# Kernel tuning notes

Measured on AMD Instinct MI355X. Metric: run time of the kernel, lower is better.

Reference implementation:

```python
import jax, jax.numpy as jnp
import numpy as np

K = 3
K2 = K * K


def conv2d(x, w, b, stride=1, pad=0):
    y = jax.lax.conv_general_dilated(
        x, w, (stride, stride), [(pad, pad), (pad, pad)],
        dimension_numbers=('NCHW', 'OIHW', 'NCHW'))
    return y + b[None, :, None, None]


def bilinear_gather(x, ys, xs):
    # x: [B,C,H,W]; ys,xs: [B,K2,H,W] float coords; zero outside bounds (torchvision deform_conv2d semantics)
    B, C, H, W = x.shape
    y0 = jnp.floor(ys)
    x0 = jnp.floor(xs)
    fy = (ys - y0)[:, None]  # [B,1,K2,H,W]
    fx = (xs - x0)[:, None]
    xf = x.reshape(B, C, H * W)

    def gather(yc, xc):
        valid = (yc >= 0) & (yc <= H - 1) & (xc >= 0) & (xc <= W - 1)
        yi = jnp.clip(yc, 0, H - 1).astype(jnp.int32)
        xi = jnp.clip(xc, 0, W - 1).astype(jnp.int32)
        idx = (yi * W + xi).reshape(B, 1, -1)
        g = jnp.take_along_axis(xf, idx, axis=2).reshape(B, C, K2, H, W)
        return g * valid[:, None].astype(x.dtype)

    g00 = gather(y0, x0)
    g01 = gather(y0, x0 + 1)
    g10 = gather(y0 + 1, x0)
    g11 = gather(y0 + 1, x0 + 1)
    return (g00 * (1 - fy) * (1 - fx) + g01 * (1 - fy) * fx
            + g10 * fy * (1 - fx) + g11 * fy * fx)


def deform_conv(x, w_off, b_off, w, b):
    # DCNv1: offsets predicted by a regular 3x3 conv, then 3x3 conv over bilinearly sampled taps
    B, C, H, W = x.shape
    pad = 1
    off = conv2d(x, w_off, b_off, pad=pad).reshape(B, K2, 2, H, W)  # (dy,dx) per tap
    ky, kx = jnp.meshgrid(jnp.arange(K), jnp.arange(K), indexing='ij')
    base_y = jnp.arange(H)[None, None, :, None] + (ky.reshape(K2) - pad)[None, :, None, None]
    base_x = jnp.arange(W)[None, None, None, :] + (kx.reshape(K2) - pad)[None, :, None, None]
    ys = base_y + off[:, :, 0]
    xs = base_x + off[:, :, 1]
    samples = bilinear_gather(x, ys, xs)  # [B,C,K2,H,W]
    out = jnp.einsum('bckhw,ock->bohw', samples, w.reshape(w.shape[0], C, K2))
    return out + b[None, :, None, None]


def band_high_mask(h, w):
    y, x = jnp.meshgrid(jnp.arange(h), jnp.arange(w), indexing='ij')
    d = jnp.sqrt(((y - h // 2) ** 2 + (x - w // 2) ** 2).astype(jnp.float32))
    return (d > h // 16).astype(jnp.float32)


def reference(x, w1, b1, ws, bs, wb, bb, woff, boff, wreg, breg, w2, b2):
    B, Cin, Hx, Wx = x.shape
    c0 = conv2d(x, w1, b1)                                  # 1x1 reduce
    c1 = conv2d(c0, ws, bs, stride=2, pad=0)                # 3x3 s2 p0 -> 111x111
    c1 = jax.lax.reduce_window(c1, -jnp.inf, jax.lax.max,
                               (1, 1, 7, 7), (1, 1, 3, 3), 'VALID')  # -> 35x35
    f = jnp.fft.fftshift(jnp.fft.fft2(c1, axes=(-2, -1)), axes=(-2, -1))
    mag = jnp.abs(f)
    phase = jnp.angle(f)
    h, w = mag.shape[-2], mag.shape[-1]
    hb = mag * band_high_mask(h, w)
    for l in range(3):  # fixed structural loop over the 3 DCN+ReLU blocks
        hb = jax.nn.relu(deform_conv(hb, woff[l], boff[l], wreg[l], breg[l]))
    rec = jax.lax.complex(hb * jnp.cos(phase), hb * jnp.sin(phase))
    rec = jnp.real(jnp.fft.ifft2(jnp.fft.ifftshift(rec, axes=(-2, -1)), axes=(-2, -1)))
    up = jax.image.resize(rec, (B, rec.shape[1], Hx, Wx), method='bilinear')  # align_corners=False
    c2 = jax.nn.sigmoid(conv2d(conv2d(c0, wb, bb) + up, w2, b2))
    return x * c2


def setup_inputs():
    key = jax.random.key(0)
    ks = jax.random.split(key, 8)
    B, Cin, H, W = 4, 256, 224, 224
    Cr = Cin // 8
    f32 = jnp.float32
    x = jax.random.normal(ks[0], (B, Cin, H, W), f32)
    w1 = jax.random.normal(ks[1], (Cr, Cin, 1, 1), f32) * 0.05
    b1 = jnp.zeros((Cr,), f32)
    ws = jax.random.normal(ks[2], (Cr, Cr, 3, 3), f32) * 0.05
    bs = jnp.zeros((Cr,), f32)
    wb = jax.random.normal(ks[3], (Cr, Cr, 1, 1), f32) * 0.05
    bb = jnp.zeros((Cr,), f32)
    woff = jax.random.normal(ks[4], (3, 2 * K2, Cr, 3, 3), f32) * 0.002  # small -> moderate offsets
    boff = jnp.zeros((3, 2 * K2), f32)
    wreg = jax.random.normal(ks[5], (3, Cr, Cr, 3, 3), f32) * 0.05
    breg = jnp.zeros((3, Cr), f32)
    w2 = jax.random.normal(ks[6], (Cin, Cr, 1, 1), f32) * 0.05
    b2 = jnp.zeros((Cin,), f32)
    return dict(x=x, w1=w1, b1=b1, ws=ws, bs=bs, wb=wb, bb=bb,
                woff=woff, boff=boff, wreg=wreg, breg=breg, w2=w2, b2=b2)
```

## Files before the change

### kernel.cpp

```cpp
#include <hip/hip_runtime.h>
#include <math.h>

#define PI_F 3.14159265358979323846f

#define BATCH 4
#define CIN 256
#define CR 32
#define H0 224
#define HW0 (224*224)
#define H1 111
#define HW1 (111*111)
#define HS 35
#define HWS (35*35)

typedef short bf16x8 __attribute__((ext_vector_type(8)));
typedef float f32x4 __attribute__((ext_vector_type(4)));
typedef unsigned int u32x4 __attribute__((ext_vector_type(4)));

__device__ inline unsigned pack2(float a, float b) {
  unsigned ua = __builtin_bit_cast(unsigned, a);
  unsigned ub = __builtin_bit_cast(unsigned, b);
  return ((ua + 0x8000u) >> 16) | (((ub + 0x8000u) >> 16) << 16);
}

__device__ inline bf16x8 pack8(const float f[8]) {
  u32x4 u;
  u[0] = pack2(f[0], f[1]);
  u[1] = pack2(f[2], f[3]);
  u[2] = pack2(f[4], f[5]);
  u[3] = pack2(f[6], f[7]);
  return __builtin_bit_cast(bf16x8, u);
}

__global__ __launch_bounds__(256) void k_prep(
    const float* __restrict__ w1, const float* __restrict__ b1,
    const float* __restrict__ wb, const float* __restrict__ bb,
    float* __restrict__ Wcat, float* __restrict__ bias_v) {
  __shared__ float wbl[32 * 32];
  int t = threadIdx.x;
  for (int i = t; i < 1024; i += 256) wbl[i] = wb[i];
  __syncthreads();
  float col[32];
#pragma unroll
  for (int m = 0; m < 32; ++m) col[m] = w1[m * CIN + t];
#pragma unroll
  for (int o = 0; o < 32; ++o) {
    float s = 0.f;
#pragma unroll
    for (int m = 0; m < 32; ++m) s = fmaf(wbl[o * 32 + m], col[m], s);
    Wcat[o * CIN + t] = s;
  }
  if (t < 32) {
    float s = bb[t];
#pragma unroll
    for (int m = 0; m < 32; ++m) s = fmaf(wbl[t * 32 + m], b1[m], s);
    bias_v[t] = s;
  }
}

__global__ __launch_bounds__(256) void k_conv1x1(
    const float* __restrict__ x, const float* __restrict__ w1,
    const float* __restrict__ b1, const float* __restrict__ Wcat,
    const float* __restrict__ bias_v,
    float* __restrict__ c0, float* __restrict__ v0) {
  int tid = threadIdx.x, lane = tid & 63, wid = tid >> 6;
  int l15 = lane & 15, lg = lane >> 4;
  int pxg = blockIdx.x * 256 + wid * 64;
  int b = pxg / HW0, p0 = pxg % HW0;
  f32x4 acc[4][4];
#pragma unroll
  for (int ct = 0; ct < 4; ++ct)
#pragma unroll
    for (int pt = 0; pt < 4; ++pt)
#pragma unroll
      for (int r = 0; r < 4; ++r) acc[ct][pt][r] = 0.f;
  const float* xb = x + (size_t)b * CIN * HW0 + p0 + l15;
  for (int ks = 0; ks < 8; ++ks) {
    bf16x8 Bf[4];
#pragma unroll
    for (int pt = 0; pt < 4; ++pt) {
      const float* xp = xb + (size_t)(ks * 32 + lg * 8) * HW0 + pt * 16;
      float f[8];
#pragma unroll
      for (int j = 0; j < 8; ++j) f[j] = xp[(size_t)j * HW0];
      Bf[pt] = pack8(f);
    }
    bf16x8 A[4];
#pragma unroll
    for (int ct = 0; ct < 4; ++ct) {
      const float* base = (ct < 2)
          ? w1 + (ct * 16 + l15) * CIN
          : Wcat + ((ct - 2) * 16 + l15) * CIN;
      const float* wr = base + ks * 32 + lg * 8;
      float f[8];
      float4 a0 = *reinterpret_cast<const float4*>(wr);
      float4 a1 = *reinterpret_cast<const float4*>(wr + 4);
      f[0]=a0.x; f[1]=a0.y; f[2]=a0.z; f[3]=a0.w;
      f[4]=a1.x; f[5]=a1.y; f[6]=a1.z; f[7]=a1.w;
      A[ct] = pack8(f);
    }
#pragma unroll
    for (int ct = 0; ct < 4; ++ct)
#pragma unroll
      for (int pt = 0; pt < 4; ++pt)
        acc[ct][pt] = __builtin_amdgcn_mfma_f32_16x16x32_bf16(
            Bf[pt], A[ct], acc[ct][pt], 0, 0, 0);
  }
#pragma unroll
  for (int ct = 0; ct < 4; ++ct) {
    int co = (ct & 1) * 16 + l15;
    float bias = (ct < 2) ? b1[co] : bias_v[co];
    float* dst = (ct < 2) ? c0 : v0;
    float* ob = dst + ((size_t)b * CR + co) * HW0 + p0;
#pragma unroll
    for (int pt = 0; pt < 4; ++pt) {
      int pxo = pt * 16 + lg * 4;
      float4 r4 = make_float4(acc[ct][pt][0] + bias, acc[ct][pt][1] + bias,
                              acc[ct][pt][2] + bias, acc[ct][pt][3] + bias);
      *reinterpret_cast<float4*>(ob + pxo) = r4;
    }
  }
}

#define PPR 56
#define PAIRS_B (H1 * PPR)
#define PAIRS_T (BATCH * PAIRS_B)
#define C3_THREADS (PAIRS_T * 4)
__global__ __launch_bounds__(256) void k_conv3x3s2(
    const float* __restrict__ c0, const float* __restrict__ wsw,
    const float* __restrict__ bs, float* __restrict__ c1) {
  __shared__ float wl[288 * 32];
  int tid = threadIdx.x;
  for (int i = tid; i < 9216; i += 256) {
    int o = i & 31, r = i >> 5;
    wl[i] = wsw[o * 288 + r];
  }
  __syncthreads();
  int T = blockIdx.x * 256 + tid;
  if (T >= C3_THREADS) return;
  int og = T / PAIRS_T;
  int pair = T % PAIRS_T;
  int b = pair / PAIRS_B;
  int pr = pair % PAIRS_B;
  int y = pr / PPR, xp = pr % PPR;
  bool tail = (xp == PPR - 1);
  const float* ibase = c0 + (size_t)b * CR * HW0 + (2 * y) * H0 + 4 * xp;
  float acc0[8], acc1[8];
#pragma unroll
  for (int j = 0; j < 8; ++j) { acc0[j] = 0.f; acc1[j] = 0.f; }
  for (int ci = 0; ci < CR; ++ci) {
    float p[3][5];
#pragma unroll
    for (int ky = 0; ky < 3; ++ky) {
      const float* rp = ibase + (size_t)ci * HW0 + ky * H0;
      float4 v = *reinterpret_cast<const float4*>(rp);
      p[ky][0] = v.x; p[ky][1] = v.y; p[ky][2] = v.z; p[ky][3] = v.w;
      p[ky][4] = tail ? 0.f : rp[4];
    }
    const float* wbase = &wl[ci * 9 * 32 + og * 8];
#pragma unroll
    for (int k = 0; k < 9; ++k) {
      int ky = k / 3, kx = k % 3;
      float4 wa = *reinterpret_cast<const float4*>(wbase + k * 32);
      float4 wc = *reinterpret_cast<const float4*>(wbase + k * 32 + 4);
      float wv[8] = {wa.x, wa.y, wa.z, wa.w, wc.x, wc.y, wc.z, wc.w};
      float pa = p[ky][kx], pb = p[ky][kx + 2];
#pragma unroll
      for (int j = 0; j < 8; ++j) {
        acc0[j] = fmaf(pa, wv[j], acc0[j]);
        acc1[j] = fmaf(pb, wv[j], acc1[j]);
      }
    }
  }
  float* ob = c1 + (size_t)b * CR * HW1 + y * H1 + 2 * xp;
  int o0 = og * 8;
#pragma unroll
  for (int j = 0; j < 8; ++j) {
    float bias = bs[o0 + j];
    ob[(size_t)(o0 + j) * HW1] = acc0[j] + bias;
    if (!tail) ob[(size_t)(o0 + j) * HW1 + 1] = acc1[j] + bias;
  }
}

__global__ __launch_bounds__(512) void k_fft(
    const float* __restrict__ c1, float* __restrict__ hb,
    float* __restrict__ cph, float* __restrict__ sph) {
  __shared__ float p[HWS];
  __shared__ float Tr[HWS], Ti[HWS];
  __shared__ float twc[HS], tws[HS];
  int img = blockIdx.x;
  const float* cb = c1 + (size_t)img * HW1;
  for (int i = threadIdx.x; i < HWS; i += 512) {
    int y = i / HS, x = i % HS;
    const float* ip = cb + (3 * y) * H1 + 3 * x;
    float m = -INFINITY;
#pragma unroll
    for (int ky = 0; ky < 7; ++ky)
#pragma unroll
      for (int kx = 0; kx < 7; ++kx)
        m = fmaxf(m, ip[ky * H1 + kx]);
    p[i] = m;
  }
  if (threadIdx.x < HS) {
    float ang = -2.f * PI_F * (float)threadIdx.x / (float)HS;
    twc[threadIdx.x] = cosf(ang);
    tws[threadIdx.x] = sinf(ang);
  }
  __syncthreads();
  for (int i = threadIdx.x; i < HWS; i += 512) {
    int u = i / HS, xx = i % HS;
    float sr = 0.f, si = 0.f;
    int t = 0;
    for (int y = 0; y < HS; ++y) {
      float v = p[y * HS + xx];
      sr = fmaf(v, twc[t], sr);
      si = fmaf(v, tws[t], si);
      t += u; if (t >= HS) t -= HS;
    }
    Tr[i] = sr; Ti[i] = si;
  }
  __syncthreads();
  float* hp = hb + (size_t)img * HWS;
  float* cp = cph + (size_t)img * HWS;
  float* sp = sph + (size_t)img * HWS;
  for (int i = threadIdx.x; i < HWS; i += 512) {
    int oy = i / HS, ox = i % HS;
    int u = oy + 18; if (u >= HS) u -= HS;
    int v = ox + 18; if (v >= HS) v -= HS;
    float fr = 0.f, fi = 0.f;
    int t = 0;
    for (int xx = 0; xx < HS; ++xx) {
      float tr = Tr[u * HS + xx], ti = Ti[u * HS + xx];
      float c = twc[t], s = tws[t];
      fr += tr * c - ti * s;
      fi += tr * s + ti * c;
      t += v; if (t >= HS) t -= HS;
    }
    float mag = sqrtf(fr * fr + fi * fi);
    float ic = 1.f, is = 0.f;
    if (mag > 0.f) { ic = fr / mag; is = fi / mag; }
    int dy = oy - 17, dx = ox - 17;
    float m = (dy * dy + dx * dx > 4) ? 1.f : 0.f;
    hp[i] = mag * m;
    cp[i] = ic; sp[i] = is;
  }
}

__global__ __launch_bounds__(256) void k_dcn(
    const float* __restrict__ hin, float* __restrict__ hout,
    const float* __restrict__ woff, const float* __restrict__ boff,
    const float* __restrict__ wreg, const float* __restrict__ breg) {
  __shared__ float wo[18 * CR * 9];
  __shared__ float wr[CR * CR * 9];
  __shared__ float bo[18], br[CR];
  for (int i = threadIdx.x; i < 18 * CR * 9; i += 256) wo[i] = woff[i];
  for (int i = threadIdx.x; i < CR * CR * 9; i += 256) wr[i] = wreg[i];
  if (threadIdx.x < 18) bo[threadIdx.x] = boff[threadIdx.x];
  if (threadIdx.x < CR) br[threadIdx.x] = breg[threadIdx.x];
  __syncthreads();
  int pg = threadIdx.x >> 5;
  int sub = threadIdx.x & 31;
  int pid = blockIdx.x * 8 + pg;
  bool active = pid < BATCH * HWS;
  int b = pid / HWS, r = pid % HWS;
  int y = r / HS, x = r % HS;
  const float* ib = hin + (size_t)b * CR * HWS;
  float off[18];
#pragma unroll
  for (int j = 0; j < 18; ++j) off[j] = 0.f;
  if (active) {
    const float* ip = ib + (size_t)sub * HWS;
#pragma unroll
    for (int ky = 0; ky < 3; ++ky) {
      int yy = y + ky - 1;
      if (yy < 0 || yy > HS - 1) continue;
#pragma unroll
      for (int kx = 0; kx < 3; ++kx) {
        int xx = x + kx - 1;
        if (xx < 0 || xx > HS - 1) continue;
        float v = ip[yy * HS + xx];
#pragma unroll
        for (int j = 0; j < 18; ++j)
          off[j] = fmaf(v, wo[(j * CR + sub) * 9 + ky * 3 + kx], off[j]);
      }
    }
  }
#pragma unroll
  for (int d = 1; d < 32; d <<= 1)
#pragma unroll
    for (int j = 0; j < 18; ++j)
      off[j] += __shfl_xor(off[j], d);
#pragma unroll
  for (int j = 0; j < 18; ++j) off[j] += bo[j];
  float acc[CR];
#pragma unroll
  for (int o = 0; o < CR; ++o) acc[o] = 0.f;
  if (active) {
    const float* ip = ib + (size_t)sub * HWS;
#pragma unroll
    for (int k = 0; k < 9; ++k) {
      int ky = k / 3, kx = k % 3;
      float ysf = (float)(y + ky - 1) + off[2 * k];
      float xsf = (float)(x + kx - 1) + off[2 * k + 1];
      float y0 = floorf(ysf), x0 = floorf(xsf);
      float fy = ysf - y0, fx = xsf - x0;
      float y1 = y0 + 1.f, x1 = x0 + 1.f;
      bool vy0 = (y0 >= 0.f) && (y0 <= 34.f);
      bool vy1 = (y1 >= 0.f) && (y1 <= 34.f);
      bool vx0 = (x0 >= 0.f) && (x0 <= 34.f);
      bool vx1 = (x1 >= 0.f) && (x1 <= 34.f);
      int iy0 = (int)fminf(fmaxf(y0, 0.f), 34.f);
      int iy1 = (int)fminf(fmaxf(y1, 0.f), 34.f);
      int ix0 = (int)fminf(fmaxf(x0, 0.f), 34.f);
      int ix1 = (int)fminf(fmaxf(x1, 0.f), 34.f);
      float w00 = (vy0 && vx0) ? (1.f - fy) * (1.f - fx) : 0.f;
      float w01 = (vy0 && vx1) ? (1.f - fy) * fx : 0.f;
      float w10 = (vy1 && vx0) ? fy * (1.f - fx) : 0.f;
      float w11 = (vy1 && vx1) ? fy * fx : 0.f;
      float s = w00 * ip[iy0 * HS + ix0] + w01 * ip[iy0 * HS + ix1]
              + w10 * ip[iy1 * HS + ix0] + w11 * ip[iy1 * HS + ix1];
#pragma unroll
      for (int o = 0; o < CR; ++o)
        acc[o] = fmaf(s, wr[(o * CR + sub) * 9 + k], acc[o]);
    }
  }
#pragma unroll
  for (int d = 1; d < 32; d <<= 1)
#pragma unroll
    for (int o = 0; o < CR; ++o)
      acc[o] += __shfl_xor(acc[o], d);
  if (active) {
    float* ob = hout + (size_t)b * CR * HWS + r;
    float v = acc[sub] + br[sub];
    ob[(size_t)sub * HWS] = fmaxf(v, 0.f);
  }
}

__global__ __launch_bounds__(512) void k_ifft(
    const float* __restrict__ hb, const float* __restrict__ cph,
    const float* __restrict__ sph, float* __restrict__ rec) {
  __shared__ float Gr[HWS], Gi[HWS];
  __shared__ float Tr[HWS], Ti[HWS];
  __shared__ float twc[HS], tws[HS];
  int img = blockIdx.x;
  const float* hp = hb + (size_t)img * HWS;
  const float* cp = cph + (size_t)img * HWS;
  const float* sp = sph + (size_t)img * HWS;
  if (threadIdx.x < HS) {
    float ang = 2.f * PI_F * (float)threadIdx.x / (float)HS;
    twc[threadIdx.x] = cosf(ang);
    tws[threadIdx.x] = sinf(ang);
  }
  for (int i = threadIdx.x; i < HWS; i += 512) {
    int m = i / HS, n = i % HS;
    int sm = m + 17; if (sm >= HS) sm -= HS;
    int sn = n + 17; if (sn >= HS) sn -= HS;
    int si = sm * HS + sn;
    float h = hp[si];
    Gr[i] = h * cp[si];
    Gi[i] = h * sp[si];
  }
  __syncthreads();
  for (int i = threadIdx.x; i < HWS; i += 512) {
    int yy = i / HS, v = i % HS;
    float sr = 0.f, sii = 0.f;
    int t = 0;
    for (int u = 0; u < HS; ++u) {
      float gr = Gr[u * HS + v], gi = Gi[u * HS + v];
      float c = twc[t], s = tws[t];
      sr += gr * c - gi * s;
      sii += gr * s + gi * c;
      t += yy; if (t >= HS) t -= HS;
    }
    Tr[i] = sr; Ti[i] = sii;
  }
  __syncthreads();
  float* rp = rec + (size_t)img * HWS;
  const float inv = 1.f / (float)(HWS);
  for (int i = threadIdx.x; i < HWS; i += 512) {
    int yy = i / HS, xx = i % HS;
    float sr = 0.f;
    int t = 0;
    for (int v = 0; v < HS; ++v) {
      sr += Tr[yy * HS + v] * twc[t] - Ti[yy * HS + v] * tws[t];
      t += xx; if (t >= HS) t -= HS;
    }
    rp[i] = sr * inv;
  }
}

__global__ __launch_bounds__(256) void k_final(
    const float* __restrict__ x, const float* __restrict__ v0buf,
    const float* __restrict__ rec,
    const float* __restrict__ w2, const float* __restrict__ b2,
    float* __restrict__ out) {
  __shared__ unsigned Bls[64 * 20];
  int tid = threadIdx.x;
  int pxg = blockIdx.x * 64;
  int b = pxg / HW0, p0 = pxg % HW0;
  int lane = tid & 63, wid = tid >> 6;
  int l15 = lane & 15, lg = lane >> 4;
  int ctb = wid * 64;
  float4 xpre[4][4];
#pragma unroll
  for (int ct = 0; ct < 4; ++ct) {
    int co = ctb + ct * 16 + l15;
    const float* xb = x + ((size_t)b * CIN + co) * HW0 + p0;
#pragma unroll
    for (int pt = 0; pt < 4; ++pt)
      xpre[ct][pt] = *reinterpret_cast<const float4*>(xb + pt * 16 + lg * 4);
  }
  {
    int px = tid & 63, half = tid >> 6;
    int p = p0 + px;
    int h = p / H0, wc = p % H0;
    const float scale = (float)HS / (float)H0;
    float sy = ((float)h + 0.5f) * scale - 0.5f;
    float sx = ((float)wc + 0.5f) * scale - 0.5f;
    float y0f = floorf(sy), x0f = floorf(sx);
    float fy = sy - y0f, fx = sx - x0f;
    int y0 = max(0, min(HS - 1, (int)y0f));
    int y1 = max(0, min(HS - 1, (int)y0f + 1));
    int x0 = max(0, min(HS - 1, (int)x0f));
    int x1 = max(0, min(HS - 1, (int)x0f + 1));
    float w00 = (1.f - fy) * (1.f - fx), w01 = (1.f - fy) * fx;
    float w10 = fy * (1.f - fx), w11 = fy * fx;
    int i00 = y0 * HS + x0, i01 = y0 * HS + x1;
    int i10 = y1 * HS + x0, i11 = y1 * HS + x1;
    const float* rb = rec + ((size_t)b * CR + half * 8) * HWS;
    const float* vb = v0buf + ((size_t)b * CR + half * 8) * HW0 + p;
    float f[8];
#pragma unroll
    for (int j = 0; j < 8; ++j) {
      const float* rp = rb + (size_t)j * HWS;
      float u = w00 * rp[i00] + w01 * rp[i01] + w10 * rp[i10] + w11 * rp[i11];
      f[j] = vb[(size_t)j * HW0] + u;
    }
    u32x4 u4;
    u4[0] = pack2(f[0], f[1]);
    u4[1] = pack2(f[2], f[3]);
    u4[2] = pack2(f[4], f[5]);
    u4[3] = pack2(f[6], f[7]);
    *reinterpret_cast<u32x4*>(&Bls[px * 20 + half * 4]) = u4;
  }
  __syncthreads();
  bf16x8 Bf[4];
#pragma unroll
  for (int pt = 0; pt < 4; ++pt) {
    u32x4 u4 = *reinterpret_cast<const u32x4*>(&Bls[(pt * 16 + l15) * 20 + lg * 4]);
    Bf[pt] = __builtin_bit_cast(bf16x8, u4);
  }
  bf16x8 A[4];
#pragma unroll
  for (int ct = 0; ct < 4; ++ct) {
    const float* wr = w2 + (ctb + ct * 16 + l15) * CR + lg * 8;
    float f[8];
    float4 a0 = *reinterpret_cast<const float4*>(wr);
    float4 a1 = *reinterpret_cast<const float4*>(wr + 4);
    f[0]=a0.x; f[1]=a0.y; f[2]=a0.z; f[3]=a0.w;
    f[4]=a1.x; f[5]=a1.y; f[6]=a1.z; f[7]=a1.w;
    A[ct] = pack8(f);
  }
  f32x4 acc[4][4];
#pragma unroll
  for (int ct = 0; ct < 4; ++ct)
#pragma unroll
    for (int pt = 0; pt < 4; ++pt)
#pragma unroll
      for (int r = 0; r < 4; ++r) acc[ct][pt][r] = 0.f;
#pragma unroll
  for (int ct = 0; ct < 4; ++ct)
#pragma unroll
    for (int pt = 0; pt < 4; ++pt)
      acc[ct][pt] = __builtin_amdgcn_mfma_f32_16x16x32_bf16(
          Bf[pt], A[ct], acc[ct][pt], 0, 0, 0);
#pragma unroll
  for (int ct = 0; ct < 4; ++ct) {
    int co = ctb + ct * 16 + l15;
    float bias = b2[co];
    float* ob = out + ((size_t)b * CIN + co) * HW0 + p0;
#pragma unroll
    for (int pt = 0; pt < 4; ++pt) {
      int pxo = pt * 16 + lg * 4;
      float4 x4 = xpre[ct][pt];
      float s0 = acc[ct][pt][0] + bias;
      float s1 = acc[ct][pt][1] + bias;
      float s2 = acc[ct][pt][2] + bias;
      float s3 = acc[ct][pt][3] + bias;
      float4 r4;
      r4.x = x4.x * __builtin_amdgcn_rcpf(1.f + __expf(-s0));
      r4.y = x4.y * __builtin_amdgcn_rcpf(1.f + __expf(-s1));
      r4.z = x4.z * __builtin_amdgcn_rcpf(1.f + __expf(-s2));
      r4.w = x4.w * __builtin_amdgcn_rcpf(1.f + __expf(-s3));
      *reinterpret_cast<float4*>(ob + pxo) = r4;
    }
  }
}

extern "C" void kernel_launch(void* const* d_in, const int* in_sizes, int n_in,
                              void* d_out, int out_size, void* d_ws, size_t ws_size,
                              hipStream_t stream) {
  const float* x    = (const float*)d_in[0];
  const float* w1   = (const float*)d_in[1];
  const float* b1   = (const float*)d_in[2];
  const float* wsw  = (const float*)d_in[3];
  const float* bs   = (const float*)d_in[4];
  const float* wb   = (const float*)d_in[5];
  const float* bb   = (const float*)d_in[6];
  const float* woff = (const float*)d_in[7];
  const float* boff = (const float*)d_in[8];
  const float* wreg = (const float*)d_in[9];
  const float* breg = (const float*)d_in[10];
  const float* w2   = (const float*)d_in[11];
  const float* b2   = (const float*)d_in[12];
  float* out = (float*)d_out;

  float* ws_f = (float*)d_ws;
  float* c0   = ws_f;
  float* v0   = c0 + (size_t)BATCH * CR * HW0;
  float* c1   = v0 + (size_t)BATCH * CR * HW0;
  float* hbA  = c1 + (size_t)BATCH * CR * HW1;
  float* hbB  = hbA + (size_t)BATCH * CR * HWS;
  float* cph  = hbB + (size_t)BATCH * CR * HWS;
  float* sph  = cph + (size_t)BATCH * CR * HWS;
  float* rec  = sph + (size_t)BATCH * CR * HWS;
  float* Wcat = rec + (size_t)BATCH * CR * HWS;
  float* bias_v = Wcat + 32 * CIN;

  k_prep<<<1, 256, 0, stream>>>(w1, b1, wb, bb, Wcat, bias_v);
  k_conv1x1<<<BATCH * HW0 / 256, 256, 0, stream>>>(x, w1, b1, Wcat, bias_v, c0, v0);
  k_conv3x3s2<<<(C3_THREADS + 255) / 256, 256, 0, stream>>>(c0, wsw, bs, c1);
  k_fft<<<BATCH * CR, 512, 0, stream>>>(c1, hbA, cph, sph);
  k_dcn<<<(BATCH * HWS + 7) / 8, 256, 0, stream>>>(hbA, hbB, woff, boff, wreg, breg);
  k_dcn<<<(BATCH * HWS + 7) / 8, 256, 0, stream>>>(hbB, hbA, woff + 5184, boff + 18, wreg + 9216, breg + 32);
  k_dcn<<<(BATCH * HWS + 7) / 8, 256, 0, stream>>>(hbA, hbB, woff + 2 * 5184, boff + 36, wreg + 2 * 9216, breg + 64);
  k_ifft<<<BATCH * CR, 512, 0, stream>>>(hbB, cph, sph, rec);
  dim3 gf(BATCH * HW0 / 64, 1);
  k_final<<<gf, 256, 0, stream>>>(x, v0, rec, w2, b2, out);
}
```

Baseline: 331.6 us.

## Fuse FFT, three DCN layers and IFFT into one cooperative persistent kernel

Replaces five separate launches (forward DFT, three deformable conv layers, inverse DFT) with a single cooperative kernel of 256 blocks that uses grid-wide syncs between stages. The DFT stages are split across two blocks per image by row halves, and the DCN stage uses a grid-stride loop over pixels. This removes per-launch overhead and tail gaps between small kernels. In exchange, each block redundantly recomputes the max-pool and first DFT pass, the DCN phase has less parallelism (256 blocks instead of about 613), and grid syncs add their own cost.

```diff
diff --git a/kernel.cpp b/kernel.cpp
--- a/kernel.cpp
+++ b/kernel.cpp
@@ -1,5 +1,8 @@
 #include <hip/hip_runtime.h>
+#include <hip/hip_cooperative_groups.h>
 #include <math.h>
+
+namespace cg = cooperative_groups;
 
 #define PI_F 3.14159265358979323846f
 
@@ -182,210 +185,235 @@
   }
 }
 
-__global__ __launch_bounds__(512) void k_fft(
-    const float* __restrict__ c1, float* __restrict__ hb,
-    float* __restrict__ cph, float* __restrict__ sph) {
-  __shared__ float p[HWS];
-  __shared__ float Tr[HWS], Ti[HWS];
-  __shared__ float twc[HS], tws[HS];
-  int img = blockIdx.x;
-  const float* cb = c1 + (size_t)img * HW1;
-  for (int i = threadIdx.x; i < HWS; i += 512) {
-    int y = i / HS, x = i % HS;
-    const float* ip = cb + (3 * y) * H1 + 3 * x;
-    float m = -INFINITY;
-#pragma unroll
-    for (int ky = 0; ky < 7; ++ky)
-#pragma unroll
-      for (int kx = 0; kx < 7; ++kx)
-        m = fmaxf(m, ip[ky * H1 + kx]);
-    p[i] = m;
-  }
-  if (threadIdx.x < HS) {
-    float ang = -2.f * PI_F * (float)threadIdx.x / (float)HS;
-    twc[threadIdx.x] = cosf(ang);
-    tws[threadIdx.x] = sinf(ang);
-  }
-  __syncthreads();
-  for (int i = threadIdx.x; i < HWS; i += 512) {
-    int u = i / HS, xx = i % HS;
-    float sr = 0.f, si = 0.f;
-    int t = 0;
-    for (int y = 0; y < HS; ++y) {
-      float v = p[y * HS + xx];
-      sr = fmaf(v, twc[t], sr);
-      si = fmaf(v, tws[t], si);
-      t += u; if (t >= HS) t -= HS;
-    }
-    Tr[i] = sr; Ti[i] = si;
-  }
-  __syncthreads();
-  float* hp = hb + (size_t)img * HWS;
-  float* cp = cph + (size_t)img * HWS;
-  float* sp = sph + (size_t)img * HWS;
-  for (int i = threadIdx.x; i < HWS; i += 512) {
-    int oy = i / HS, ox = i % HS;
-    int u = oy + 18; if (u >= HS) u -= HS;
-    int v = ox + 18; if (v >= HS) v -= HS;
-    float fr = 0.f, fi = 0.f;
-    int t = 0;
-    for (int xx = 0; xx < HS; ++xx) {
-      float tr = Tr[u * HS + xx], ti = Ti[u * HS + xx];
-      float c = twc[t], s = tws[t];
-      fr += tr * c - ti * s;
-      fi += tr * s + ti * c;
-      t += v; if (t >= HS) t -= HS;
-    }
-    float mag = sqrtf(fr * fr + fi * fi);
-    float ic = 1.f, is = 0.f;
-    if (mag > 0.f) { ic = fr / mag; is = fi / mag; }
-    int dy = oy - 17, dx = ox - 17;
-    float m = (dy * dy + dx * dx > 4) ? 1.f : 0.f;
-    hp[i] = mag * m;
-    cp[i] = ic; sp[i] = is;
-  }
-}
-
-__global__ __launch_bounds__(256) void k_dcn(
-    const float* __restrict__ hin, float* __restrict__ hout,
+#define MIDB 256
+__global__ __launch_bounds__(256) void k_mid(
+    const float* __restrict__ c1,
     const float* __restrict__ woff, const float* __restrict__ boff,
-    const float* __restrict__ wreg, const float* __restrict__ breg) {
-  __shared__ float wo[18 * CR * 9];
-  __shared__ float wr[CR * CR * 9];
-  __shared__ float bo[18], br[CR];
-  for (int i = threadIdx.x; i < 18 * CR * 9; i += 256) wo[i] = woff[i];
-  for (int i = threadIdx.x; i < CR * CR * 9; i += 256) wr[i] = wreg[i];
-  if (threadIdx.x < 18) bo[threadIdx.x] = boff[threadIdx.x];
-  if (threadIdx.x < CR) br[threadIdx.x] = breg[threadIdx.x];
-  __syncthreads();
-  int pg = threadIdx.x >> 5;
-  int sub = threadIdx.x & 31;
-  int pid = blockIdx.x * 8 + pg;
-  bool active = pid < BATCH * HWS;
-  int b = pid / HWS, r = pid % HWS;
-  int y = r / HS, x = r % HS;
-  const float* ib = hin + (size_t)b * CR * HWS;
-  float off[18];
-#pragma unroll
-  for (int j = 0; j < 18; ++j) off[j] = 0.f;
-  if (active) {
-    const float* ip = ib + (size_t)sub * HWS;
-#pragma unroll
-    for (int ky = 0; ky < 3; ++ky) {
-      int yy = y + ky - 1;
-      if (yy < 0 || yy > HS - 1) continue;
-#pragma unroll
-      for (int kx = 0; kx < 3; ++kx) {
-        int xx = x + kx - 1;
-        if (xx < 0 || xx > HS - 1) continue;
-        float v = ip[yy * HS + xx];
+    const float* __restrict__ wreg, const float* __restrict__ breg,
+    float* __restrict__ hbA, float* __restrict__ hbB,
+    float* __restrict__ cph, float* __restrict__ sph,
+    float* __restrict__ rec) {
+  __shared__ float sm[14464];
+  cg::grid_group gridg = cg::this_grid();
+  int tid = threadIdx.x;
+  int blk = blockIdx.x;
+
+  {
+    float* p  = sm;
+    float* Tr = sm + 2450;
+    float* Ti = sm + 3675;
+    float* twc = sm + 4900;
+    float* tws = sm + 4935;
+    int img = blk >> 1, half = blk & 1;
+    int ub = half ? 0 : 18;
+    int un = half ? 18 : 17;
+    int oyb = half ? 17 : 0;
+    const float* cb = c1 + (size_t)img * HW1;
+    for (int i = tid; i < HWS; i += 256) {
+      int y = i / HS, x = i % HS;
+      const float* ip = cb + (3 * y) * H1 + 3 * x;
+      float m = -INFINITY;
+#pragma unroll
+      for (int ky = 0; ky < 7; ++ky)
+#pragma unroll
+        for (int kx = 0; kx < 7; ++kx)
+          m = fmaxf(m, ip[ky * H1 + kx]);
+      p[i] = m;
+    }
+    if (tid < HS) {
+      float ang = -2.f * PI_F * (float)tid / (float)HS;
+      twc[tid] = cosf(ang);
+      tws[tid] = sinf(ang);
+    }
+    __syncthreads();
+    for (int i = tid; i < un * HS; i += 256) {
+      int u = ub + i / HS, xx = i % HS;
+      float sr = 0.f, si = 0.f;
+      int t = 0;
+      for (int y = 0; y < HS; ++y) {
+        float v = p[y * HS + xx];
+        sr = fmaf(v, twc[t], sr);
+        si = fmaf(v, tws[t], si);
+        t += u; if (t >= HS) t -= HS;
+      }
+      Tr[u * HS + xx] = sr; Ti[u * HS + xx] = si;
+    }
+    __syncthreads();
+    float* hp = hbA + (size_t)img * HWS;
+    float* cp = cph + (size_t)img * HWS;
+    float* sp = sph + (size_t)img * HWS;
+    for (int i = tid; i < un * HS; i += 256) {
+      int oy = oyb + i / HS, ox = i % HS;
+      int u = oy + 18; if (u >= HS) u -= HS;
+      int v = ox + 18; if (v >= HS) v -= HS;
+      float fr = 0.f, fi = 0.f;
+      int t = 0;
+      for (int xx = 0; xx < HS; ++xx) {
+        float tr = Tr[u * HS + xx], ti = Ti[u * HS + xx];
+        float c = twc[t], s = tws[t];
+        fr += tr * c - ti * s;
+        fi += tr * s + ti * c;
+        t += v; if (t >= HS) t -= HS;
+      }
+      float mag = sqrtf(fr * fr + fi * fi);
+      float ic = 1.f, is = 0.f;
+      if (mag > 0.f) { ic = fr / mag; is = fi / mag; }
+      int dy = oy - 17, dx = ox - 17;
+      float m = (dy * dy + dx * dx > 4) ? 1.f : 0.f;
+      int o = oy * HS + ox;
+      hp[o] = mag * m;
+      cp[o] = ic; sp[o] = is;
+    }
+  }
+  gridg.sync();
+
+  for (int l = 0; l < 3; ++l) {
+    const float* hin = (l & 1) ? hbB : hbA;
+    float* hout = (l & 1) ? hbA : hbB;
+    float* wo = sm;
+    float* wr = sm + 5184;
+    float* bo = sm + 14400;
+    float* br = sm + 14432;
+    const float* wofL = woff + l * 5184;
+    const float* wrgL = wreg + l * 9216;
+    for (int i = tid; i < 5184; i += 256) wo[i] = wofL[i];
+    for (int i = tid; i < 9216; i += 256) wr[i] = wrgL[i];
+    if (tid < 18) bo[tid] = boff[l * 18 + tid];
+    if (tid < 32) br[tid] = breg[l * 32 + tid];
+    __syncthreads();
+    int pg = tid >> 5;
+    int sub = tid & 31;
+    for (int pid = blk * 8 + pg; pid < BATCH * HWS; pid += MIDB * 8) {
+      int b = pid / HWS, r = pid % HWS;
+      int y = r / HS, x = r % HS;
+      const float* ib = hin + (size_t)b * CR * HWS;
+      float off[18];
+#pragma unroll
+      for (int j = 0; j < 18; ++j) off[j] = 0.f;
+      {
+        const float* ip = ib + (size_t)sub * HWS;
+#pragma unroll
+        for (int ky = 0; ky < 3; ++ky) {
+          int yy = y + ky - 1;
+          if (yy < 0 || yy > HS - 1) continue;
+#pragma unroll
+          for (int kx = 0; kx < 3; ++kx) {
+            int xx = x + kx - 1;
+            if (xx < 0 || xx > HS - 1) continue;
+            float v = ip[yy * HS + xx];
+#pragma unroll
+            for (int j = 0; j < 18; ++j)
+              off[j] = fmaf(v, wo[(j * CR + sub) * 9 + ky * 3 + kx], off[j]);
+          }
+        }
+      }
+#pragma unroll
+      for (int d = 1; d < 32; d <<= 1)
 #pragma unroll
         for (int j = 0; j < 18; ++j)
-          off[j] = fmaf(v, wo[(j * CR + sub) * 9 + ky * 3 + kx], off[j]);
-      }
-    }
-  }
-#pragma unroll
-  for (int d = 1; d < 32; d <<= 1)
-#pragma unroll
-    for (int j = 0; j < 18; ++j)
-      off[j] += __shfl_xor(off[j], d);
-#pragma unroll
-  for (int j = 0; j < 18; ++j) off[j] += bo[j];
-  float acc[CR];
-#pragma unroll
-  for (int o = 0; o < CR; ++o) acc[o] = 0.f;
-  if (active) {
-    const float* ip = ib + (size_t)sub * HWS;
-#pragma unroll
-    for (int k = 0; k < 9; ++k) {
-      int ky = k / 3, kx = k % 3;
-      float ysf = (float)(y + ky - 1) + off[2 * k];
-      float xsf = (float)(x + kx - 1) + off[2 * k + 1];
-      float y0 = floorf(ysf), x0 = floorf(xsf);
-      float fy = ysf - y0, fx = xsf - x0;
-      float y1 = y0 + 1.f, x1 = x0 + 1.f;
-      bool vy0 = (y0 >= 0.f) && (y0 <= 34.f);
-      bool vy1 = (y1 >= 0.f) && (y1 <= 34.f);
-      bool vx0 = (x0 >= 0.f) && (x0 <= 34.f);
-      bool vx1 = (x1 >= 0.f) && (x1 <= 34.f);
-      int iy0 = (int)fminf(fmaxf(y0, 0.f), 34.f);
-      int iy1 = (int)fminf(fmaxf(y1, 0.f), 34.f);
-      int ix0 = (int)fminf(fmaxf(x0, 0.f), 34.f);
-      int ix1 = (int)fminf(fmaxf(x1, 0.f), 34.f);
-      float w00 = (vy0 && vx0) ? (1.f - fy) * (1.f - fx) : 0.f;
-      float w01 = (vy0 && vx1) ? (1.f - fy) * fx : 0.f;
-      float w10 = (vy1 && vx0) ? fy * (1.f - fx) : 0.f;
-      float w11 = (vy1 && vx1) ? fy * fx : 0.f;
-      float s = w00 * ip[iy0 * HS + ix0] + w01 * ip[iy0 * HS + ix1]
-              + w10 * ip[iy1 * HS + ix0] + w11 * ip[iy1 * HS + ix1];
-#pragma unroll
-      for (int o = 0; o < CR; ++o)
-        acc[o] = fmaf(s, wr[(o * CR + sub) * 9 + k], acc[o]);
-    }
-  }
-#pragma unroll
-  for (int d = 1; d < 32; d <<= 1)
-#pragma unroll
-    for (int o = 0; o < CR; ++o)
-      acc[o] += __shfl_xor(acc[o], d);
-  if (active) {
-    float* ob = hout + (size_t)b * CR * HWS + r;
-    float v = acc[sub] + br[sub];
-    ob[(size_t)sub * HWS] = fmaxf(v, 0.f);
-  }
-}
-
-__global__ __launch_bounds__(512) void k_ifft(
-    const float* __restrict__ hb, const float* __restrict__ cph,
-    const float* __restrict__ sph, float* __restrict__ rec) {
-  __shared__ float Gr[HWS], Gi[HWS];
-  __shared__ float Tr[HWS], Ti[HWS];
-  __shared__ float twc[HS], tws[HS];
-  int img = blockIdx.x;
-  const float* hp = hb + (size_t)img * HWS;
-  const float* cp = cph + (size_t)img * HWS;
-  const float* sp = sph + (size_t)img * HWS;
-  if (threadIdx.x < HS) {
-    float ang = 2.f * PI_F * (float)threadIdx.x / (float)HS;
-    twc[threadIdx.x] = cosf(ang);
-    tws[threadIdx.x] = sinf(ang);
-  }
-  for (int i = threadIdx.x; i < HWS; i += 512) {
-    int m = i / HS, n = i % HS;
-    int sm = m + 17; if (sm >= HS) sm -= HS;
-    int sn = n + 17; if (sn >= HS) sn -= HS;
-    int si = sm * HS + sn;
-    float h = hp[si];
-    Gr[i] = h * cp[si];
-    Gi[i] = h * sp[si];
-  }
-  __syncthreads();
-  for (int i = threadIdx.x; i < HWS; i += 512) {
-    int yy = i / HS, v = i % HS;
-    float sr = 0.f, sii = 0.f;
-    int t = 0;
-    for (int u = 0; u < HS; ++u) {
-      float gr = Gr[u * HS + v], gi = Gi[u * HS + v];
-      float c = twc[t], s = tws[t];
-      sr += gr * c - gi * s;
-      sii += gr * s + gi * c;
-      t += yy; if (t >= HS) t -= HS;
-    }
-    Tr[i] = sr; Ti[i] = sii;
-  }
-  __syncthreads();
-  float* rp = rec + (size_t)img * HWS;
-  const float inv = 1.f / (float)(HWS);
-  for (int i = threadIdx.x; i < HWS; i += 512) {
-    int yy = i / HS, xx = i % HS;
-    float sr = 0.f;
-    int t = 0;
-    for (int v = 0; v < HS; ++v) {
-      sr += Tr[yy * HS + v] * twc[t] - Ti[yy * HS + v] * tws[t];
-      t += xx; if (t >= HS) t -= HS;
-    }
-    rp[i] = sr * inv;
+          off[j] += __shfl_xor(off[j], d);
+#pragma unroll
+      for (int j = 0; j < 18; ++j) off[j] += bo[j];
+      float acc[CR];
+#pragma unroll
+      for (int o = 0; o < CR; ++o) acc[o] = 0.f;
+      {
+        const float* ip = ib + (size_t)sub * HWS;
+#pragma unroll
+        for (int k = 0; k < 9; ++k) {
+          int ky = k / 3, kx = k % 3;
+          float ysf = (float)(y + ky - 1) + off[2 * k];
+          float xsf = (float)(x + kx - 1) + off[2 * k + 1];
+          float y0 = floorf(ysf), x0 = floorf(xsf);
+          float fy = ysf - y0, fx = xsf - x0;
+          float y1 = y0 + 1.f, x1 = x0 + 1.f;
+          bool vy0 = (y0 >= 0.f) && (y0 <= 34.f);
+          bool vy1 = (y1 >= 0.f) && (y1 <= 34.f);
+          bool vx0 = (x0 >= 0.f) && (x0 <= 34.f);
+          bool vx1 = (x1 >= 0.f) && (x1 <= 34.f);
+          int iy0 = (int)fminf(fmaxf(y0, 0.f), 34.f);
+          int iy1 = (int)fminf(fmaxf(y1, 0.f), 34.f);
+          int ix0 = (int)fminf(fmaxf(x0, 0.f), 34.f);
+          int ix1 = (int)fminf(fmaxf(x1, 0.f), 34.f);
+          float w00 = (vy0 && vx0) ? (1.f - fy) * (1.f - fx) : 0.f;
+          float w01 = (vy0 && vx1) ? (1.f - fy) * fx : 0.f;
+          float w10 = (vy1 && vx0) ? fy * (1.f - fx) : 0.f;
+          float w11 = (vy1 && vx1) ? fy * fx : 0.f;
+          float s = w00 * ip[iy0 * HS + ix0] + w01 * ip[iy0 * HS + ix1]
+                  + w10 * ip[iy1 * HS + ix0] + w11 * ip[iy1 * HS + ix1];
+#pragma unroll
+          for (int o = 0; o < CR; ++o)
+            acc[o] = fmaf(s, wr[(o * CR + sub) * 9 + k], acc[o]);
+        }
+      }
+#pragma unroll
+      for (int d = 1; d < 32; d <<= 1)
+#pragma unroll
+        for (int o = 0; o < CR; ++o)
+          acc[o] += __shfl_xor(acc[o], d);
+      {
+        float* ob = hout + (size_t)b * CR * HWS + r;
+        float v = acc[sub] + br[sub];
+        ob[(size_t)sub * HWS] = fmaxf(v, 0.f);
+      }
+    }
+    gridg.sync();
+  }
+
+  {
+    float* Gr = sm;
+    float* Gi = sm + 1225;
+    float* Tr = sm + 2450;
+    float* Ti = sm + 3675;
+    float* twc = sm + 4900;
+    float* tws = sm + 4935;
+    int img = blk >> 1, half = blk & 1;
+    int yb = half ? 18 : 0;
+    int yn = half ? 17 : 18;
+    const float* hp = hbB + (size_t)img * HWS;
+    const float* cp = cph + (size_t)img * HWS;
+    const float* sp = sph + (size_t)img * HWS;
+    if (tid < HS) {
+      float ang = 2.f * PI_F * (float)tid / (float)HS;
+      twc[tid] = cosf(ang);
+      tws[tid] = sinf(ang);
+    }
+    for (int i = tid; i < HWS; i += 256) {
+      int m = i / HS, n = i % HS;
+      int smi = m + 17; if (smi >= HS) smi -= HS;
+      int sn = n + 17; if (sn >= HS) sn -= HS;
+      int si = smi * HS + sn;
+      float h = hp[si];
+      Gr[i] = h * cp[si];
+      Gi[i] = h * sp[si];
+    }
+    __syncthreads();
+    for (int i = tid; i < yn * HS; i += 256) {
+      int yy = yb + i / HS, v = i % HS;
+      float sr = 0.f, sii = 0.f;
+      int t = 0;
+      for (int u = 0; u < HS; ++u) {
+        float gr = Gr[u * HS + v], gi = Gi[u * HS + v];
+        float c = twc[t], s = tws[t];
+        sr += gr * c - gi * s;
+        sii += gr * s + gi * c;
+        t += yy; if (t >= HS) t -= HS;
+      }
+      Tr[yy * HS + v] = sr; Ti[yy * HS + v] = sii;
+    }
+    __syncthreads();
+    float* rp = rec + (size_t)img * HWS;
+    const float inv = 1.f / (float)(HWS);
+    for (int i = tid; i < yn * HS; i += 256) {
+      int yy = yb + i / HS, xx = i % HS;
+      float sr = 0.f;
+      int t = 0;
+      for (int v = 0; v < HS; ++v) {
+        sr += Tr[yy * HS + v] * twc[t] - Ti[yy * HS + v] * tws[t];
+        t += xx; if (t >= HS) t -= HS;
+      }
+      rp[yy * HS + xx] = sr * inv;
+    }
   }
 }
 
@@ -530,11 +558,12 @@
   k_prep<<<1, 256, 0, stream>>>(w1, b1, wb, bb, Wcat, bias_v);
   k_conv1x1<<<BATCH * HW0 / 256, 256, 0, stream>>>(x, w1, b1, Wcat, bias_v, c0, v0);
   k_conv3x3s2<<<(C3_THREADS + 255) / 256, 256, 0, stream>>>(c0, wsw, bs, c1);
-  k_fft<<<BATCH * CR, 512, 0, stream>>>(c1, hbA, cph, sph);
-  k_dcn<<<(BATCH * HWS + 7) / 8, 256, 0, stream>>>(hbA, hbB, woff, boff, wreg, breg);
-  k_dcn<<<(BATCH * HWS + 7) / 8, 256, 0, stream>>>(hbB, hbA, woff + 5184, boff + 18, wreg + 9216, breg + 32);
-  k_dcn<<<(BATCH * HWS + 7) / 8, 256, 0, stream>>>(hbA, hbB, woff + 2 * 5184, boff + 36, wreg + 2 * 9216, breg + 64);
-  k_ifft<<<BATCH * CR, 512, 0, stream>>>(hbB, cph, sph, rec);
+
+  void* margs[] = { (void*)&c1, (void*)&woff, (void*)&boff, (void*)&wreg,
+                    (void*)&breg, (void*)&hbA, (void*)&hbB, (void*)&cph,
+                    (void*)&sph, (void*)&rec };
+  hipLaunchCooperativeKernel((void*)k_mid, dim3(MIDB), dim3(256), margs, 0, stream);
+
   dim3 gf(BATCH * HW0 / 64, 1);
   k_final<<<gf, 256, 0, stream>>>(x, v0, rec, w2, b2, out);
 }
```

Measured after the change: 454.1 us. 36.9% more time.
